# Kernel optimization log

Measured on AMD Instinct MI355X. Metric: run time of the kernel, lower is better.

Reference implementation:

```python
import jax, jax.numpy as jnp
import numpy as np

# attn_reps = "8x0n+30x1n": per head channel C = 8 scalars + 30 Lorentz four-vectors (4 each) = 128
N_SCALARS, N_VECTORS = 8, 30
ETA = jnp.diag(jnp.array([1.0, -1.0, -1.0, -1.0], dtype=jnp.float32))  # Minkowski metric


def _quat_to_rot(q):
    # q: (M,4) unit quaternions -> (M,3,3) rotation matrices
    w, x, y, z = q[:, 0], q[:, 1], q[:, 2], q[:, 3]
    r0 = jnp.stack([1 - 2 * (y * y + z * z), 2 * (x * y - w * z), 2 * (x * z + w * y)], axis=-1)
    r1 = jnp.stack([2 * (x * y + w * z), 1 - 2 * (x * x + z * z), 2 * (y * z - w * x)], axis=-1)
    r2 = jnp.stack([2 * (x * z - w * y), 2 * (y * z + w * x), 1 - 2 * (x * x + y * y)], axis=-1)
    return jnp.stack([r0, r1, r2], axis=-2)


def _random_lorentz(key, M):
    # random proper Lorentz transforms: boost(beta) @ blockdiag(1, R)
    k1, k2 = jax.random.split(key)
    quat = jax.random.normal(k1, (M, 4), dtype=jnp.float32)
    quat = quat / jnp.linalg.norm(quat, axis=-1, keepdims=True)
    R = _quat_to_rot(quat)  # (M,3,3)
    beta = jax.random.uniform(k2, (M, 3), minval=-1.0, maxval=1.0, dtype=jnp.float32) * (0.6 / np.sqrt(3.0))
    b2 = jnp.sum(beta * beta, axis=-1)  # (M,), < 0.36
    gamma = 1.0 / jnp.sqrt(1.0 - b2)
    n = beta / jnp.sqrt(jnp.maximum(b2, 1e-12))[:, None]
    gb = gamma[:, None] * beta  # (M,3)
    top = jnp.concatenate([gamma[:, None], gb], axis=-1)[:, None, :]  # (M,1,4)
    spatial = jnp.eye(3, dtype=jnp.float32) + (gamma - 1.0)[:, None, None] * n[:, :, None] * n[:, None, :]
    bottom = jnp.concatenate([gb[:, :, None], spatial], axis=-1)  # (M,3,4)
    B = jnp.concatenate([top, bottom], axis=-2)  # (M,4,4) boost
    rot4 = jnp.zeros((M, 4, 4), dtype=jnp.float32).at[:, 0, 0].set(1.0).at[:, 1:, 1:].set(R)
    return jnp.einsum('mij,mjk->mik', B, rot4)


def setup_inputs() -> dict:
    key = jax.random.key(0)
    kq, kk, kv, kl = jax.random.split(key, 4)
    B, H, N, C = 8, 8, 1024, 128
    q = jax.random.normal(kq, (B, H, N, C), dtype=jnp.float32)
    k = jax.random.normal(kk, (B, H, N, C), dtype=jnp.float32)
    v = jax.random.normal(kv, (B, H, N, C), dtype=jnp.float32)
    L = _random_lorentz(kl, B * N).reshape(B, N, 4, 4)
    return {"q_local": q, "k_local": k, "v_local": v, "lframes_matrices": L}


def _transform(x, M):
    # TensorRepsTransform: scalars pass through, four-vectors get v' = M v (per particle)
    # x: (B,H,N,C), M: (B,N,4,4)
    s = x[..., :N_SCALARS]
    vec = x[..., N_SCALARS:].reshape(x.shape[:-1] + (N_VECTORS, 4))
    vec = jnp.einsum('bnij,bhnvj->bhnvi', M, vec)
    return jnp.concatenate([s, vec.reshape(x.shape[:-1] + (N_VECTORS * 4,))], axis=-1)


def reference(q_local, k_local, v_local, lframes_matrices):
    C = q_local.shape[-1]
    # InverseLFrames: Lorentz inverse  Lambda^{-1} = eta Lambda^T eta
    inv = jnp.einsum('ij,bnkj,kl->bnil', ETA, lframes_matrices, ETA)
    # LowerIndices: lower the output index -> eta @ Lambda^{-1}
    lower_inv = jnp.einsum('ij,bnjk->bnik', ETA, inv)
    q_g = _transform(q_local, inv)
    k_g = _transform(k_local, lower_inv)
    v_g = _transform(v_local, inv)
    # standard SDPA (scale 1/sqrt(C))
    scores = jnp.einsum('bhqc,bhkc->bhqk', q_g, k_g) * (1.0 / np.sqrt(C))
    attn = jax.nn.softmax(scores, axis=-1)
    out_g = jnp.einsum('bhqk,bhkc->bhqc', attn, v_g)
    # back to local frame with Lambda itself
    return _transform(out_g, lframes_matrices)
```

## Files before the change

### kernel.cpp

```cpp
#include <hip/hip_runtime.h>

typedef _Float16 f16;
typedef _Float16 f16x4 __attribute__((ext_vector_type(4)));
typedef _Float16 f16x8 __attribute__((ext_vector_type(8)));
typedef float    f32x4 __attribute__((ext_vector_type(4)));

#define NSEQ 1024
#define CD   128
#define QT   128
#define KT   128

__global__ __launch_bounds__(256)
void ipa_pre(const float* __restrict__ qg, const float* __restrict__ kg,
             const float* __restrict__ vg, const float* __restrict__ Lm,
             f16* __restrict__ qh, f16* __restrict__ kh, f16* __restrict__ vh)
{
    __shared__ float LL[64 * 16];
    const int bh = blockIdx.x, nt = blockIdx.y, b = bh >> 3, tid = threadIdx.x;
    const float* Lb = Lm + ((size_t)b * NSEQ + nt * 64) * 16;
    for (int t = tid; t < 64 * 16; t += 256) LL[t] = Lb[t];
    __syncthreads();
    const size_t base = ((size_t)bh * NSEQ + nt * 64) * CD;
    const float sc = 0.08838834764831845f;
    #pragma unroll
    for (int it = 0; it < 8; ++it) {
        int g = it * 256 + tid;
        int row = g >> 5, cg = g & 31;
        size_t idx = base + row * CD + cg * 4;
        const float* Lr = &LL[row * 16];
        float4 xq = *(const float4*)(qg + idx);
        float4 xk = *(const float4*)(kg + idx);
        float4 xv = *(const float4*)(vg + idx);
        float4 yq = xq, yk = xk, yv = xv;
        if (cg >= 2) {
            float t0 = xk.x, t1 = -xk.y, t2 = -xk.z, t3 = -xk.w;
            yk.x = Lr[0]*t0 + Lr[4]*t1 + Lr[8] *t2 + Lr[12]*t3;
            yk.y = Lr[1]*t0 + Lr[5]*t1 + Lr[9] *t2 + Lr[13]*t3;
            yk.z = Lr[2]*t0 + Lr[6]*t1 + Lr[10]*t2 + Lr[14]*t3;
            yk.w = Lr[3]*t0 + Lr[7]*t1 + Lr[11]*t2 + Lr[15]*t3;
            t0 = xv.x; t1 = -xv.y; t2 = -xv.z; t3 = -xv.w;
            yv.x =  (Lr[0]*t0 + Lr[4]*t1 + Lr[8] *t2 + Lr[12]*t3);
            yv.y = -(Lr[1]*t0 + Lr[5]*t1 + Lr[9] *t2 + Lr[13]*t3);
            yv.z = -(Lr[2]*t0 + Lr[6]*t1 + Lr[10]*t2 + Lr[14]*t3);
            yv.w = -(Lr[3]*t0 + Lr[7]*t1 + Lr[11]*t2 + Lr[15]*t3);
            t0 = xq.x; t1 = -xq.y; t2 = -xq.z; t3 = -xq.w;
            yq.x =  (Lr[0]*t0 + Lr[4]*t1 + Lr[8] *t2 + Lr[12]*t3);
            yq.y = -(Lr[1]*t0 + Lr[5]*t1 + Lr[9] *t2 + Lr[13]*t3);
            yq.z = -(Lr[2]*t0 + Lr[6]*t1 + Lr[10]*t2 + Lr[14]*t3);
            yq.w = -(Lr[3]*t0 + Lr[7]*t1 + Lr[11]*t2 + Lr[15]*t3);
        }
        f16x4 hq = {(f16)(yq.x*sc), (f16)(yq.y*sc), (f16)(yq.z*sc), (f16)(yq.w*sc)};
        f16x4 hk = {(f16)yk.x, (f16)yk.y, (f16)yk.z, (f16)yk.w};
        f16x4 hv = {(f16)yv.x, (f16)yv.y, (f16)yv.z, (f16)yv.w};
        *(f16x4*)(qh + idx) = hq;
        *(f16x4*)(kh + idx) = hk;
        *(f16x4*)(vh + idx) = hv;
    }
}

__global__ __launch_bounds__(256, 2)
void ipa_attn(const f16* __restrict__ qh, const f16* __restrict__ kh,
              const f16* __restrict__ vh, const float* __restrict__ Lm,
              float* __restrict__ out)
{
    __shared__ __align__(16) f16 Ks[KT * CD];
    __shared__ __align__(16) f16 Vt[CD * KT];

    const int tid  = threadIdx.x;
    const int bh   = blockIdx.x, qt = blockIdx.y, b = bh >> 3;
    const int lane = tid & 63, w = tid >> 6, lq = lane & 15, quad = lane >> 4;
    const int q0   = qt * QT;
    const size_t kvbase = (size_t)bh * NSEQ * CD;

    f16x8 qf[2][4];
    #pragma unroll
    for (int u = 0; u < 2; ++u)
        #pragma unroll
        for (int cs = 0; cs < 4; ++cs)
            qf[u][cs] = *(const f16x8*)(qh + kvbase + (size_t)(q0 + w*32 + u*16 + lq) * CD
                                           + cs * 32 + quad * 8);

    f32x4 oacc[2][8];
    #pragma unroll
    for (int u = 0; u < 2; ++u)
        #pragma unroll
        for (int cb = 0; cb < 8; ++cb) oacc[u][cb] = (f32x4){0.f, 0.f, 0.f, 0.f};
    float mrun[2] = {-1e30f, -1e30f}, lrun[2] = {0.f, 0.f};

    for (int kt0 = 0; kt0 < NSEQ; kt0 += KT) {
        __syncthreads();

        #pragma unroll
        for (int it = 0; it < 8; ++it) {
            int g = it * 256 + tid;
            int m = g >> 4, c0 = (g & 15) * 8;
            int mm = m & 31, h = (mm >> 4) & 1, a = (mm >> 2) & 3, r = mm & 3;
            int kap = (m & ~31) | (8 * a + 4 * h + r);
            f16x8 kv = *(const f16x8*)(kh + kvbase + (size_t)(kt0 + kap) * CD + c0);
            *(f16x8*)&Ks[m * CD + (c0 ^ ((m & 7) << 3))] = kv;
        }
        #pragma unroll
        for (int j = 0; j < 8; ++j) {
            int key = (tid & 63) + (j & 1) * 64;
            int c0  = (tid >> 6) * 32 + (j >> 1) * 8;
            f16x8 vv = *(const f16x8*)(vh + kvbase + (size_t)(kt0 + key) * CD + c0);
            #pragma unroll
            for (int i = 0; i < 8; ++i)
                Vt[(c0 + i) * KT + (key ^ (i << 3))] = vv[i];
        }
        __syncthreads();

        #pragma unroll
        for (int half = 0; half < 2; ++half) {
            const int kb = half * 64;
            f32x4 s[2][4];
            #pragma unroll
            for (int u = 0; u < 2; ++u)
                #pragma unroll
                for (int g = 0; g < 4; ++g) s[u][g] = (f32x4){0.f, 0.f, 0.f, 0.f};
            #pragma unroll
            for (int g = 0; g < 4; ++g) {
                int R = kb + g * 16 + lq;
                #pragma unroll
                for (int cs = 0; cs < 4; ++cs) {
                    f16x8 ka = *(const f16x8*)&Ks[R * CD + ((cs*32 + quad*8) ^ ((R & 7) << 3))];
                    s[0][g] = __builtin_amdgcn_mfma_f32_16x16x32_f16(ka, qf[0][cs], s[0][g], 0, 0, 0);
                    s[1][g] = __builtin_amdgcn_mfma_f32_16x16x32_f16(ka, qf[1][cs], s[1][g], 0, 0, 0);
                }
            }
            f16x8 pf[2][2];
            float alpha[2];
            #pragma unroll
            for (int u = 0; u < 2; ++u) {
                float mx = -1e30f;
                #pragma unroll
                for (int g = 0; g < 4; ++g)
                    mx = fmaxf(mx, fmaxf(fmaxf(s[u][g].x, s[u][g].y), fmaxf(s[u][g].z, s[u][g].w)));
                mx = fmaxf(mx, __shfl_xor(mx, 16, 64));
                mx = fmaxf(mx, __shfl_xor(mx, 32, 64));
                float mnew = fmaxf(mrun[u], mx);
                alpha[u] = __expf(mrun[u] - mnew);
                float rs = 0.f;
                float p[16];
                #pragma unroll
                for (int g = 0; g < 4; ++g) {
                    p[g*4+0] = __expf(s[u][g].x - mnew);
                    p[g*4+1] = __expf(s[u][g].y - mnew);
                    p[g*4+2] = __expf(s[u][g].z - mnew);
                    p[g*4+3] = __expf(s[u][g].w - mnew);
                    rs += (p[g*4+0] + p[g*4+1]) + (p[g*4+2] + p[g*4+3]);
                }
                rs += __shfl_xor(rs, 16, 64);
                rs += __shfl_xor(rs, 32, 64);
                lrun[u] = alpha[u] * lrun[u] + rs;
                mrun[u] = mnew;
                pf[u][0] = (f16x8){(f16)p[0],(f16)p[1],(f16)p[2],(f16)p[3],(f16)p[4],(f16)p[5],(f16)p[6],(f16)p[7]};
                pf[u][1] = (f16x8){(f16)p[8],(f16)p[9],(f16)p[10],(f16)p[11],(f16)p[12],(f16)p[13],(f16)p[14],(f16)p[15]};
            }
            #pragma unroll
            for (int u = 0; u < 2; ++u)
                #pragma unroll
                for (int cb = 0; cb < 8; ++cb) oacc[u][cb] *= alpha[u];
            #pragma unroll
            for (int p2 = 0; p2 < 2; ++p2) {
                int kbase = kb + p2 * 32 + quad * 8;
                #pragma unroll
                for (int cb = 0; cb < 8; ++cb) {
                    int c = cb * 16 + lq;
                    f16x8 vf = *(const f16x8*)&Vt[c * KT + (kbase ^ ((c & 7) << 3))];
                    oacc[0][cb] = __builtin_amdgcn_mfma_f32_16x16x32_f16(vf, pf[0][p2], oacc[0][cb], 0, 0, 0);
                    oacc[1][cb] = __builtin_amdgcn_mfma_f32_16x16x32_f16(vf, pf[1][p2], oacc[1][cb], 0, 0, 0);
                }
            }
        }
    }

    #pragma unroll
    for (int u = 0; u < 2; ++u) {
        const int qrow = w * 32 + u * 16 + lq;
        float invl = 1.0f / lrun[u];
        const float* Lr = Lm + ((size_t)b * NSEQ + q0 + qrow) * 16;
        float* ob = out + ((size_t)bh * NSEQ + q0 + qrow) * CD;
        #pragma unroll
        for (int cb = 0; cb < 8; ++cb) {
            int c0 = cb * 16 + quad * 4;
            float o0 = oacc[u][cb].x*invl, o1 = oacc[u][cb].y*invl;
            float o2 = oacc[u][cb].z*invl, o3 = oacc[u][cb].w*invl;
            float4 r;
            if (c0 >= 8) {
                r.x = Lr[0] *o0 + Lr[1] *o1 + Lr[2] *o2 + Lr[3] *o3;
                r.y = Lr[4] *o0 + Lr[5] *o1 + Lr[6] *o2 + Lr[7] *o3;
                r.z = Lr[8] *o0 + Lr[9] *o1 + Lr[10]*o2 + Lr[11]*o3;
                r.w = Lr[12]*o0 + Lr[13]*o1 + Lr[14]*o2 + Lr[15]*o3;
            } else {
                r.x = o0; r.y = o1; r.z = o2; r.w = o3;
            }
            *(float4*)(ob + c0) = r;
        }
    }
}

extern "C" void kernel_launch(void* const* d_in, const int* in_sizes, int n_in,
                              void* d_out, int out_size, void* d_ws, size_t ws_size,
                              hipStream_t stream) {
    const float* q = (const float*)d_in[0];
    const float* k = (const float*)d_in[1];
    const float* v = (const float*)d_in[2];
    const float* L = (const float*)d_in[3];
    float* o = (float*)d_out;
    const size_t tot = (size_t)64 * NSEQ * CD;
    f16* qh = (f16*)d_ws;
    f16* kh = qh + tot;
    f16* vh = kh + tot;
    dim3 grid1(64, NSEQ / 64);
    ipa_pre<<<grid1, 256, 0, stream>>>(q, k, v, L, qh, kh, vh);
    dim3 grid2(64, NSEQ / QT);
    ipa_attn<<<grid2, 256, 0, stream>>>(qh, kh, vh, L, o);
}
```

Baseline: 211.5 us.

## Pre-swizzle K/V into MFMA fragment layout and drop LDS staging in attention

```diff
diff --git a/kernel.cpp b/kernel.cpp
--- a/kernel.cpp
+++ b/kernel.cpp
@@ -1,4 +1,5 @@
 #include <hip/hip_runtime.h>
+#include <math.h>
 
 typedef _Float16 f16;
 typedef _Float16 f16x4 __attribute__((ext_vector_type(4)));
@@ -7,31 +8,33 @@
 
 #define NSEQ 1024
 #define CD   128
-#define QT   128
-#define KT   128
+#define LT   136
+
 
 __global__ __launch_bounds__(256)
-void ipa_pre(const float* __restrict__ qg, const float* __restrict__ kg,
-             const float* __restrict__ vg, const float* __restrict__ Lm,
-             f16* __restrict__ qh, f16* __restrict__ kh, f16* __restrict__ vh)
+void ipa_pre(const float* __restrict__ kg, const float* __restrict__ vg,
+             const float* __restrict__ Lm, f16* __restrict__ khs, f16* __restrict__ vhs)
 {
     __shared__ float LL[64 * 16];
-    const int bh = blockIdx.x, nt = blockIdx.y, b = bh >> 3, tid = threadIdx.x;
+    __shared__ __align__(16) f16 Kt[64 * LT];
+    __shared__ __align__(16) f16 Vt[64 * LT];
+    const int bx = blockIdx.x, nt = blockIdx.y, tid = threadIdx.x;
+    const int bh = ((bx & 7) << 3) | (bx >> 3);
+    const int b  = bh >> 3;
     const float* Lb = Lm + ((size_t)b * NSEQ + nt * 64) * 16;
     for (int t = tid; t < 64 * 16; t += 256) LL[t] = Lb[t];
     __syncthreads();
+
     const size_t base = ((size_t)bh * NSEQ + nt * 64) * CD;
-    const float sc = 0.08838834764831845f;
     #pragma unroll
     for (int it = 0; it < 8; ++it) {
         int g = it * 256 + tid;
         int row = g >> 5, cg = g & 31;
         size_t idx = base + row * CD + cg * 4;
         const float* Lr = &LL[row * 16];
-        float4 xq = *(const float4*)(qg + idx);
         float4 xk = *(const float4*)(kg + idx);
         float4 xv = *(const float4*)(vg + idx);
-        float4 yq = xq, yk = xk, yv = xv;
+        float4 yk = xk, yv = xv;
         if (cg >= 2) {
             float t0 = xk.x, t1 = -xk.y, t2 = -xk.z, t3 = -xk.w;
             yk.x = Lr[0]*t0 + Lr[4]*t1 + Lr[8] *t2 + Lr[12]*t3;
@@ -43,42 +46,88 @@
             yv.y = -(Lr[1]*t0 + Lr[5]*t1 + Lr[9] *t2 + Lr[13]*t3);
             yv.z = -(Lr[2]*t0 + Lr[6]*t1 + Lr[10]*t2 + Lr[14]*t3);
             yv.w = -(Lr[3]*t0 + Lr[7]*t1 + Lr[11]*t2 + Lr[15]*t3);
-            t0 = xq.x; t1 = -xq.y; t2 = -xq.z; t3 = -xq.w;
-            yq.x =  (Lr[0]*t0 + Lr[4]*t1 + Lr[8] *t2 + Lr[12]*t3);
-            yq.y = -(Lr[1]*t0 + Lr[5]*t1 + Lr[9] *t2 + Lr[13]*t3);
-            yq.z = -(Lr[2]*t0 + Lr[6]*t1 + Lr[10]*t2 + Lr[14]*t3);
-            yq.w = -(Lr[3]*t0 + Lr[7]*t1 + Lr[11]*t2 + Lr[15]*t3);
-        }
-        f16x4 hq = {(f16)(yq.x*sc), (f16)(yq.y*sc), (f16)(yq.z*sc), (f16)(yq.w*sc)};
+        }
         f16x4 hk = {(f16)yk.x, (f16)yk.y, (f16)yk.z, (f16)yk.w};
         f16x4 hv = {(f16)yv.x, (f16)yv.y, (f16)yv.z, (f16)yv.w};
-        *(f16x4*)(qh + idx) = hq;
-        *(f16x4*)(kh + idx) = hk;
-        *(f16x4*)(vh + idx) = hv;
+        *(f16x4*)&Kt[row * LT + cg * 4] = hk;
+        *(f16x4*)&Vt[row * LT + cg * 4] = hv;
+    }
+    __syncthreads();
+
+    f16* kout = khs + (size_t)bh * 131072 + (size_t)nt * 4 * 4 * 512;
+    #pragma unroll
+    for (int it = 0; it < 4; ++it) {
+        int slot = it * 256 + tid;
+        int g16l = slot >> 8, cs = (slot >> 6) & 3, L = slot & 63;
+        int lq = L & 15, quad = L >> 4;
+        int keyl = ((g16l >> 1) << 5) + ((lq >> 2) << 3) + ((g16l & 1) << 2) + (lq & 3);
+        f16x8 kv = *(const f16x8*)&Kt[keyl * LT + cs * 32 + quad * 8];
+        *(f16x8*)(kout + (g16l * 4 + cs) * 512 + L * 8) = kv;
+    }
+    f16* vout = vhs + (size_t)bh * 131072 + (size_t)nt * 2 * 8 * 512;
+    #pragma unroll
+    for (int it = 0; it < 4; ++it) {
+        int slot = it * 256 + tid;
+        int k32l = slot >> 9, cb = (slot >> 6) & 7, L = slot & 63;
+        int lq = L & 15, quad = L >> 4;
+        int c = cb * 16 + lq;
+        f16x8 o;
+        #pragma unroll
+        for (int j = 0; j < 8; ++j)
+            o[j] = Vt[(k32l * 32 + quad * 8 + j) * LT + c];
+        *(f16x8*)(vout + (k32l * 8 + cb) * 512 + L * 8) = o;
     }
 }
 
-__global__ __launch_bounds__(256, 2)
-void ipa_attn(const f16* __restrict__ qh, const f16* __restrict__ kh,
-              const f16* __restrict__ vh, const float* __restrict__ Lm,
+__global__ __launch_bounds__(128, 2)
+void ipa_attn(const float* __restrict__ qg, const f16* __restrict__ khs,
+              const f16* __restrict__ vhs, const float* __restrict__ Lm,
               float* __restrict__ out)
 {
-    __shared__ __align__(16) f16 Ks[KT * CD];
-    __shared__ __align__(16) f16 Vt[CD * KT];
-
-    const int tid  = threadIdx.x;
-    const int bh   = blockIdx.x, qt = blockIdx.y, b = bh >> 3;
-    const int lane = tid & 63, w = tid >> 6, lq = lane & 15, quad = lane >> 4;
-    const int q0   = qt * QT;
-    const size_t kvbase = (size_t)bh * NSEQ * CD;
+    const int n = blockIdx.x;
+    const int bh = ((n & 7) << 3) | ((n >> 3) & 7);
+    const int b  = bh >> 3;
+    const int tid = threadIdx.x;
+    const int w = tid >> 6, lane = tid & 63, lq = lane & 15, quad = lane >> 4;
+    const int qw = (n >> 6) * 2 + w;
+    const int q0 = qw * 32;
+    const f16* kbh = khs + (size_t)bh * 131072;
+    const f16* vbh = vhs + (size_t)bh * 131072;
+    const float sc2 = 0.12751744154226873f;
 
     f16x8 qf[2][4];
     #pragma unroll
-    for (int u = 0; u < 2; ++u)
-        #pragma unroll
-        for (int cs = 0; cs < 4; ++cs)
-            qf[u][cs] = *(const f16x8*)(qh + kvbase + (size_t)(q0 + w*32 + u*16 + lq) * CD
-                                           + cs * 32 + quad * 8);
+    for (int u = 0; u < 2; ++u) {
+        int qrow = q0 + u * 16 + lq;
+        const float* Lr = Lm + ((size_t)b * NSEQ + qrow) * 16;
+        const float* qp = qg + ((size_t)bh * NSEQ + qrow) * CD;
+        float Lv[16];
+        #pragma unroll
+        for (int i = 0; i < 4; ++i) *(float4*)&Lv[i*4] = *(const float4*)(Lr + i*4);
+        #pragma unroll
+        for (int cs = 0; cs < 4; ++cs) {
+            int c0 = cs * 32 + quad * 8;
+            float4 x0 = *(const float4*)(qp + c0);
+            float4 x1 = *(const float4*)(qp + c0 + 4);
+            if (c0 >= 8) {
+                float t0 = x0.x, t1 = -x0.y, t2 = -x0.z, t3 = -x0.w;
+                float4 y;
+                y.x =  (Lv[0]*t0 + Lv[4]*t1 + Lv[8] *t2 + Lv[12]*t3);
+                y.y = -(Lv[1]*t0 + Lv[5]*t1 + Lv[9] *t2 + Lv[13]*t3);
+                y.z = -(Lv[2]*t0 + Lv[6]*t1 + Lv[10]*t2 + Lv[14]*t3);
+                y.w = -(Lv[3]*t0 + Lv[7]*t1 + Lv[11]*t2 + Lv[15]*t3);
+                x0 = y;
+                t0 = x1.x; t1 = -x1.y; t2 = -x1.z; t3 = -x1.w;
+                y.x =  (Lv[0]*t0 + Lv[4]*t1 + Lv[8] *t2 + Lv[12]*t3);
+                y.y = -(Lv[1]*t0 + Lv[5]*t1 + Lv[9] *t2 + Lv[13]*t3);
+                y.z = -(Lv[2]*t0 + Lv[6]*t1 + Lv[10]*t2 + Lv[14]*t3);
+                y.w = -(Lv[3]*t0 + Lv[7]*t1 + Lv[11]*t2 + Lv[15]*t3);
+                x1 = y;
+            }
+            qf[u][cs] = (f16x8){(f16)(x0.x*sc2), (f16)(x0.y*sc2), (f16)(x0.z*sc2), (f16)(x0.w*sc2),
+                                (f16)(x1.x*sc2), (f16)(x1.y*sc2), (f16)(x1.z*sc2), (f16)(x1.w*sc2)};
+        }
+    }
 
     f32x4 oacc[2][8];
     #pragma unroll
@@ -87,100 +136,83 @@
         for (int cb = 0; cb < 8; ++cb) oacc[u][cb] = (f32x4){0.f, 0.f, 0.f, 0.f};
     float mrun[2] = {-1e30f, -1e30f}, lrun[2] = {0.f, 0.f};
 
-    for (int kt0 = 0; kt0 < NSEQ; kt0 += KT) {
-        __syncthreads();
-
-        #pragma unroll
-        for (int it = 0; it < 8; ++it) {
-            int g = it * 256 + tid;
-            int m = g >> 4, c0 = (g & 15) * 8;
-            int mm = m & 31, h = (mm >> 4) & 1, a = (mm >> 2) & 3, r = mm & 3;
-            int kap = (m & ~31) | (8 * a + 4 * h + r);
-            f16x8 kv = *(const f16x8*)(kh + kvbase + (size_t)(kt0 + kap) * CD + c0);
-            *(f16x8*)&Ks[m * CD + (c0 ^ ((m & 7) << 3))] = kv;
-        }
-        #pragma unroll
-        for (int j = 0; j < 8; ++j) {
-            int key = (tid & 63) + (j & 1) * 64;
-            int c0  = (tid >> 6) * 32 + (j >> 1) * 8;
-            f16x8 vv = *(const f16x8*)(vh + kvbase + (size_t)(kt0 + key) * CD + c0);
-            #pragma unroll
-            for (int i = 0; i < 8; ++i)
-                Vt[(c0 + i) * KT + (key ^ (i << 3))] = vv[i];
-        }
-        __syncthreads();
-
-        #pragma unroll
-        for (int half = 0; half < 2; ++half) {
-            const int kb = half * 64;
-            f32x4 s[2][4];
-            #pragma unroll
-            for (int u = 0; u < 2; ++u)
-                #pragma unroll
-                for (int g = 0; g < 4; ++g) s[u][g] = (f32x4){0.f, 0.f, 0.f, 0.f};
+    for (int it = 0; it < 16; ++it) {
+        const f16* kp = kbh + (size_t)it * 16 * 512;
+        f16x8 kf[4][4];
+        #pragma unroll
+        for (int g = 0; g < 4; ++g)
+            #pragma unroll
+            for (int cs = 0; cs < 4; ++cs)
+                kf[g][cs] = *(const f16x8*)(kp + (g * 4 + cs) * 512 + lane * 8);
+
+        f32x4 s[2][4];
+        #pragma unroll
+        for (int u = 0; u < 2; ++u)
+            #pragma unroll
+            for (int g = 0; g < 4; ++g) s[u][g] = (f32x4){0.f, 0.f, 0.f, 0.f};
+        #pragma unroll
+        for (int g = 0; g < 4; ++g)
+            #pragma unroll
+            for (int cs = 0; cs < 4; ++cs) {
+                s[0][g] = __builtin_amdgcn_mfma_f32_16x16x32_f16(kf[g][cs], qf[0][cs], s[0][g], 0, 0, 0);
+                s[1][g] = __builtin_amdgcn_mfma_f32_16x16x32_f16(kf[g][cs], qf[1][cs], s[1][g], 0, 0, 0);
+            }
+
+        const f16* vp = vbh + (size_t)it * 2 * 8 * 512;
+        f16x8 vf[2][8];
+        #pragma unroll
+        for (int k2 = 0; k2 < 2; ++k2)
+            #pragma unroll
+            for (int cb = 0; cb < 8; ++cb)
+                vf[k2][cb] = *(const f16x8*)(vp + (k2 * 8 + cb) * 512 + lane * 8);
+
+        f16x8 pf[2][2];
+        float alpha[2];
+        #pragma unroll
+        for (int u = 0; u < 2; ++u) {
+            float mx = -1e30f;
+            #pragma unroll
+            for (int g = 0; g < 4; ++g)
+                mx = fmaxf(mx, fmaxf(fmaxf(s[u][g].x, s[u][g].y), fmaxf(s[u][g].z, s[u][g].w)));
+            mx = fmaxf(mx, __shfl_xor(mx, 16, 64));
+            mx = fmaxf(mx, __shfl_xor(mx, 32, 64));
+            float mnew = fmaxf(mrun[u], mx);
+            alpha[u] = exp2f(mrun[u] - mnew);
+            float p[16], rs = 0.f;
             #pragma unroll
             for (int g = 0; g < 4; ++g) {
-                int R = kb + g * 16 + lq;
-                #pragma unroll
-                for (int cs = 0; cs < 4; ++cs) {
-                    f16x8 ka = *(const f16x8*)&Ks[R * CD + ((cs*32 + quad*8) ^ ((R & 7) << 3))];
-                    s[0][g] = __builtin_amdgcn_mfma_f32_16x16x32_f16(ka, qf[0][cs], s[0][g], 0, 0, 0);
-                    s[1][g] = __builtin_amdgcn_mfma_f32_16x16x32_f16(ka, qf[1][cs], s[1][g], 0, 0, 0);
-                }
-            }
-            f16x8 pf[2][2];
-            float alpha[2];
-            #pragma unroll
-            for (int u = 0; u < 2; ++u) {
-                float mx = -1e30f;
-                #pragma unroll
-                for (int g = 0; g < 4; ++g)
-                    mx = fmaxf(mx, fmaxf(fmaxf(s[u][g].x, s[u][g].y), fmaxf(s[u][g].z, s[u][g].w)));
-                mx = fmaxf(mx, __shfl_xor(mx, 16, 64));
-                mx = fmaxf(mx, __shfl_xor(mx, 32, 64));
-                float mnew = fmaxf(mrun[u], mx);
-                alpha[u] = __expf(mrun[u] - mnew);
-                float rs = 0.f;
-                float p[16];
-                #pragma unroll
-                for (int g = 0; g < 4; ++g) {
-                    p[g*4+0] = __expf(s[u][g].x - mnew);
-                    p[g*4+1] = __expf(s[u][g].y - mnew);
-                    p[g*4+2] = __expf(s[u][g].z - mnew);
-                    p[g*4+3] = __expf(s[u][g].w - mnew);
-                    rs += (p[g*4+0] + p[g*4+1]) + (p[g*4+2] + p[g*4+3]);
-                }
-                rs += __shfl_xor(rs, 16, 64);
-                rs += __shfl_xor(rs, 32, 64);
-                lrun[u] = alpha[u] * lrun[u] + rs;
-                mrun[u] = mnew;
-                pf[u][0] = (f16x8){(f16)p[0],(f16)p[1],(f16)p[2],(f16)p[3],(f16)p[4],(f16)p[5],(f16)p[6],(f16)p[7]};
-                pf[u][1] = (f16x8){(f16)p[8],(f16)p[9],(f16)p[10],(f16)p[11],(f16)p[12],(f16)p[13],(f16)p[14],(f16)p[15]};
-            }
-            #pragma unroll
-            for (int u = 0; u < 2; ++u)
-                #pragma unroll
-                for (int cb = 0; cb < 8; ++cb) oacc[u][cb] *= alpha[u];
-            #pragma unroll
-            for (int p2 = 0; p2 < 2; ++p2) {
-                int kbase = kb + p2 * 32 + quad * 8;
-                #pragma unroll
-                for (int cb = 0; cb < 8; ++cb) {
-                    int c = cb * 16 + lq;
-                    f16x8 vf = *(const f16x8*)&Vt[c * KT + (kbase ^ ((c & 7) << 3))];
-                    oacc[0][cb] = __builtin_amdgcn_mfma_f32_16x16x32_f16(vf, pf[0][p2], oacc[0][cb], 0, 0, 0);
-                    oacc[1][cb] = __builtin_amdgcn_mfma_f32_16x16x32_f16(vf, pf[1][p2], oacc[1][cb], 0, 0, 0);
-                }
-            }
-        }
+                p[g*4+0] = exp2f(s[u][g].x - mnew);
+                p[g*4+1] = exp2f(s[u][g].y - mnew);
+                p[g*4+2] = exp2f(s[u][g].z - mnew);
+                p[g*4+3] = exp2f(s[u][g].w - mnew);
+                rs += (p[g*4+0] + p[g*4+1]) + (p[g*4+2] + p[g*4+3]);
+            }
+            rs += __shfl_xor(rs, 16, 64);
+            rs += __shfl_xor(rs, 32, 64);
+            lrun[u] = alpha[u] * lrun[u] + rs;
+            mrun[u] = mnew;
+            pf[u][0] = (f16x8){(f16)p[0],(f16)p[1],(f16)p[2],(f16)p[3],(f16)p[4],(f16)p[5],(f16)p[6],(f16)p[7]};
+            pf[u][1] = (f16x8){(f16)p[8],(f16)p[9],(f16)p[10],(f16)p[11],(f16)p[12],(f16)p[13],(f16)p[14],(f16)p[15]};
+        }
+        #pragma unroll
+        for (int u = 0; u < 2; ++u)
+            #pragma unroll
+            for (int cb = 0; cb < 8; ++cb) oacc[u][cb] *= alpha[u];
+        #pragma unroll
+        for (int k2 = 0; k2 < 2; ++k2)
+            #pragma unroll
+            for (int cb = 0; cb < 8; ++cb) {
+                oacc[0][cb] = __builtin_amdgcn_mfma_f32_16x16x32_f16(vf[k2][cb], pf[0][k2], oacc[0][cb], 0, 0, 0);
+                oacc[1][cb] = __builtin_amdgcn_mfma_f32_16x16x32_f16(vf[k2][cb], pf[1][k2], oacc[1][cb], 0, 0, 0);
+            }
     }
 
     #pragma unroll
     for (int u = 0; u < 2; ++u) {
-        const int qrow = w * 32 + u * 16 + lq;
+        int qrow = q0 + u * 16 + lq;
         float invl = 1.0f / lrun[u];
-        const float* Lr = Lm + ((size_t)b * NSEQ + q0 + qrow) * 16;
-        float* ob = out + ((size_t)bh * NSEQ + q0 + qrow) * CD;
+        const float* Lr = Lm + ((size_t)b * NSEQ + qrow) * 16;
+        float* ob = out + ((size_t)bh * NSEQ + qrow) * CD;
         #pragma unroll
         for (int cb = 0; cb < 8; ++cb) {
             int c0 = cb * 16 + quad * 4;
@@ -208,12 +240,9 @@
     const float* v = (const float*)d_in[2];
     const float* L = (const float*)d_in[3];
     float* o = (float*)d_out;
-    const size_t tot = (size_t)64 * NSEQ * CD;
-    f16* qh = (f16*)d_ws;
-    f16* kh = qh + tot;
-    f16* vh = kh + tot;
-    dim3 grid1(64, NSEQ / 64);
-    ipa_pre<<<grid1, 256, 0, stream>>>(q, k, v, L, qh, kh, vh);
-    dim3 grid2(64, NSEQ / QT);
-    ipa_attn<<<grid2, 256, 0, stream>>>(qh, kh, vh, L, o);
+    f16* khs = (f16*)d_ws;
+    f16* vhs = khs + (size_t)64 * 131072;
+    dim3 grid1(64, 16);
+    ipa_pre<<<grid1, 256, 0, stream>>>(k, v, L, khs, vhs);
+    ipa_attn<<<1024, 128, 0, stream>>>(q, khs, vhs, L, o);
 }
```

After: 194.0 us. 8.3% less time.
